# Performance work log

Hardware: AMD Instinct MI355X
Metric: run time of the kernel (lower is better)

The kernel has to match this reference:

```python
import jax, jax.numpy as jnp
import numpy as np

N_NODES = 100000


def _graph_conv(x, W, b, src, dst, n_nodes):
    # DGL GraphConv, norm='both', weight applied before aggregation (in>out).
    E = src.shape[0]
    ones = jnp.ones((E,), dtype=x.dtype)
    out_deg = jax.ops.segment_sum(ones, src, num_segments=n_nodes)
    in_deg = jax.ops.segment_sum(ones, dst, num_segments=n_nodes)
    out_norm = jnp.clip(out_deg, 1.0, None) ** -0.5  # [N]
    in_norm = jnp.clip(in_deg, 1.0, None) ** -0.5    # [N]
    h = (x * out_norm[:, None]) @ W                  # [N, out] dense GEMM first
    msg = h[src]                                     # gather  [E, out]
    agg = jax.ops.segment_sum(msg, dst, num_segments=n_nodes)  # scatter-add
    return agg * in_norm[:, None] + b


def setup_inputs() -> dict:
    key = jax.random.key(0)
    k1, k2, k3, k4, k5 = jax.random.split(key, 5)
    E = 1600000
    features = jax.random.normal(k1, (N_NODES, 128), dtype=jnp.float32)
    src = jax.random.randint(k2, (E,), 0, N_NODES, dtype=jnp.int64)
    dst = jax.random.randint(k3, (E,), 0, N_NODES, dtype=jnp.int64)
    W1 = jax.random.normal(k4, (128, 64), dtype=jnp.float32) * (1.0 / np.sqrt(128))
    b1 = jnp.zeros((64,), dtype=jnp.float32)
    W2 = jax.random.normal(k5, (64, 32), dtype=jnp.float32) * (1.0 / np.sqrt(64))
    b2 = jnp.zeros((32,), dtype=jnp.float32)
    return {"features": features, "src": src, "dst": dst,
            "W1": W1, "b1": b1, "W2": W2, "b2": b2}


def reference(features, src, dst, W1, b1, W2, b2):
    x = jax.nn.relu(_graph_conv(features, W1, b1, src, dst, N_NODES))
    x = _graph_conv(x, W2, b2, src, dst, N_NODES)
    return x
```

## Files before the change

kernel.cpp:

```cpp
#include <hip/hip_runtime.h>
#include <hip/hip_bf16.h>


#define BSH 7
#define BNODES 128
#define SRCMASK 0x1FFFF
#define CAP 2560
#define CHUNK 4096

__device__ __forceinline__ unsigned short f2bf(float f) {
    unsigned int u = __float_as_uint(f);
    return (unsigned short)((u + 0x7FFFu + ((u >> 16) & 1u)) >> 16);
}

__global__ __launch_bounds__(1024) void k_place(const int* __restrict__ src,
        const int* __restrict__ dst, int* __restrict__ ebuf,
        unsigned char* __restrict__ sbuf, int* __restrict__ offs,
        int* __restrict__ soffs, int E) {
    __shared__ int lh[800], s[800];
    int t = threadIdx.x;
    int e0 = blockIdx.x * CHUNK;
    int e1 = min(e0 + CHUNK, E);
    if (t < 800) lh[t] = 0;
    __syncthreads();
    for (int i = e0 + t; i < e1; i += 1024) {
        atomicAdd(&lh[dst[i] >> BSH], 0x10000);
        atomicAdd(&lh[src[i] >> BSH], 1);
    }
    __syncthreads();
    if (t < 800) s[t] = lh[t];
    __syncthreads();
    for (int o = 1; o < 800; o <<= 1) {
        int u = (t < 800 && t >= o) ? s[t - o] : 0;
        __syncthreads();
        if (t < 800) s[t] += u;
        __syncthreads();
    }
    int obase = blockIdx.x * 801;
    if (t < 800) {
        int incl = s[t], c = lh[t];
        int bd = (incl >> 16) - (c >> 16);
        int bs = (incl & 0xFFFF) - (c & 0xFFFF);
        offs[obase + t] = bd;
        soffs[obase + t] = bs;
        s[t] = (bd << 16) | bs;
    }
    if (t == 0) { offs[obase + 800] = e1 - e0; soffs[obase + 800] = e1 - e0; }
    __syncthreads();
    for (int i = e0 + t; i < e1; i += 1024) {
        int sv = src[i], d = dst[i];
        int pd = atomicAdd(&s[d >> BSH], 0x10000) >> 16;
        ebuf[e0 + pd] = sv | ((d & (BNODES - 1)) << 17);
        int ps = atomicAdd(&s[sv >> BSH], 1) & 0xFFFF;
        sbuf[e0 + ps] = (unsigned char)(sv & (BNODES - 1));
    }
}

__global__ __launch_bounds__(1024) void k_sort2(const int* __restrict__ ebuf,
        const unsigned char* __restrict__ sbuf, const int* __restrict__ offs,
        const int* __restrict__ soffs, int* __restrict__ csrc,
        int* __restrict__ ostart, int* __restrict__ oend,
        float* __restrict__ nI, float* __restrict__ nO, int n, int NBLK) {
    __shared__ int cnt[BNODES], cur[BNODES], s[BNODES], scnt[BNODES];
    __shared__ int segst[400], segen[400], sst[400], sen[400];
    int t = threadIdx.x, b = blockIdx.x;
    if (t < NBLK) {
        segst[t] = t * CHUNK + offs[t * 801 + b];
        segen[t] = t * CHUNK + offs[t * 801 + b + 1];
        sst[t]   = t * CHUNK + soffs[t * 801 + b];
        sen[t]   = t * CHUNK + soffs[t * 801 + b + 1];
    }
    if (t < BNODES) { cnt[t] = 0; scnt[t] = 0; }
    __syncthreads();
    int grp = t >> 3, ln = t & 7;
    for (int sg = grp; sg < NBLK; sg += 128) {
        int en = segen[sg];
        for (int i = segst[sg] + ln; i < en; i += 8)
            atomicAdd(&cnt[ebuf[i] >> 17], 1);
        int en2 = sen[sg];
        for (int i = sst[sg] + ln; i < en2; i += 8)
            atomicAdd(&scnt[sbuf[i]], 1);
    }
    __syncthreads();
    if (t < BNODES) s[t] = cnt[t];
    __syncthreads();
    for (int o = 1; o < BNODES; o <<= 1) {
        int u = (t < BNODES && t >= o) ? s[t - o] : 0;
        __syncthreads();
        if (t < BNODES) s[t] += u;
        __syncthreads();
    }
    if (t < BNODES) {
        int e0 = b * CAP;
        int st = e0 + s[t] - cnt[t];
        cur[t] = st;
        int g = b * BNODES + t;
        if (g < n) {
            ostart[g] = st;
            oend[g] = e0 + s[t];
            nI[g] = rsqrtf(fmaxf((float)cnt[t], 1.0f));
            nO[g] = rsqrtf(fmaxf((float)scnt[t], 1.0f));
        }
    }
    __syncthreads();
    for (int sg = grp; sg < NBLK; sg += 128) {
        int en = segen[sg];
        for (int i = segst[sg] + ln; i < en; i += 8) {
            int p = ebuf[i];
            int pos = atomicAdd(&cur[p >> 17], 1);
            csrc[pos] = p & SRCMASK;
        }
    }
}

__global__ __launch_bounds__(256) void k_gemm1(const float* __restrict__ x,
                        const float* __restrict__ W1, const float* __restrict__ nO,
                        unsigned short* __restrict__ h1, int n) {
    __shared__ float sX[64 * 132];
    __shared__ float sW[128 * 64];
    const int t = threadIdx.x;
    {
        const float4* W4 = (const float4*)W1;
        float4* sW4 = (float4*)sW;
#pragma unroll
        for (int i = 0; i < 8; i++) sW4[t + 256 * i] = W4[t + 256 * i];
    }
    const int rowbase = blockIdx.x * 64;
    {
        const float4* x4 = (const float4*)x;
        float4* sX4 = (float4*)sX;
#pragma unroll
        for (int i = 0; i < 8; i++) {
            int f = t + 256 * i;
            int row = f >> 5, kc = f & 31;
            int grow = rowbase + row;
            float4 v = make_float4(0.f, 0.f, 0.f, 0.f);
            if (grow < n) v = x4[(size_t)grow * 32 + kc];
            sX4[row * 33 + kc] = v;
        }
    }
    __syncthreads();
    const int lane = t & 63, wv = t >> 6;
    const int rg = lane >> 2, cg = lane & 3;
    const int c0 = wv * 16 + cg * 4;
    float acc[4][4] = {};
    for (int kk = 0; kk < 128; kk += 4) {
        float xr[4][4], wr[4][4];
#pragma unroll
        for (int i = 0; i < 4; i++)
            *(float4*)xr[i] = *(const float4*)&sX[(rg + 16 * i) * 132 + kk];
#pragma unroll
        for (int j = 0; j < 4; j++)
            *(float4*)wr[j] = *(const float4*)&sW[(kk + j) * 64 + c0];
#pragma unroll
        for (int j = 0; j < 4; j++)
#pragma unroll
            for (int i = 0; i < 4; i++)
#pragma unroll
                for (int c = 0; c < 4; c++)
                    acc[i][c] = fmaf(xr[i][j], wr[j][c], acc[i][c]);
    }
#pragma unroll
    for (int i = 0; i < 4; i++) {
        int grow = rowbase + rg + 16 * i;
        if (grow < n) {
            float nf = nO[grow];
            ushort4 o;
            o.x = f2bf(acc[i][0] * nf); o.y = f2bf(acc[i][1] * nf);
            o.z = f2bf(acc[i][2] * nf); o.w = f2bf(acc[i][3] * nf);
            *(ushort4*)&h1[(size_t)grow * 64 + c0] = o;
        }
    }
}

__global__ void k_agg64(const unsigned short* __restrict__ h,
                        const int* __restrict__ csrc,
                        const int* __restrict__ ostart, const int* __restrict__ oend,
                        const float* __restrict__ nI, const float* __restrict__ b1,
                        float* __restrict__ x2, int n) {
    int node = blockIdx.x * 4 + (threadIdx.x >> 6);
    int lane = threadIdx.x & 63;
    if (node >= n) return;
    int s0 = ostart[node], s1 = oend[node];
    int sub = lane >> 4;
    int c4 = (lane & 15) * 4;
    float a0 = 0.f, a1 = 0.f, a2 = 0.f, a3 = 0.f;
    float d0 = 0.f, d1 = 0.f, d2 = 0.f, d3 = 0.f;
    int e = s0;
    for (; e + 7 < s1; e += 8) {
        int p0 = csrc[e + sub];
        int p1 = csrc[e + 4 + sub];
        uint2 u0 = *(const uint2*)&h[(size_t)p0 * 64 + c4];
        uint2 u1 = *(const uint2*)&h[(size_t)p1 * 64 + c4];
        a0 += __uint_as_float(u0.x << 16);
        a1 += __uint_as_float(u0.x & 0xFFFF0000u);
        a2 += __uint_as_float(u0.y << 16);
        a3 += __uint_as_float(u0.y & 0xFFFF0000u);
        d0 += __uint_as_float(u1.x << 16);
        d1 += __uint_as_float(u1.x & 0xFFFF0000u);
        d2 += __uint_as_float(u1.y << 16);
        d3 += __uint_as_float(u1.y & 0xFFFF0000u);
    }
    for (; e < s1; e += 4) {
        if (e + sub < s1) {
            int p = csrc[e + sub];
            uint2 u = *(const uint2*)&h[(size_t)p * 64 + c4];
            a0 += __uint_as_float(u.x << 16);
            a1 += __uint_as_float(u.x & 0xFFFF0000u);
            a2 += __uint_as_float(u.y << 16);
            a3 += __uint_as_float(u.y & 0xFFFF0000u);
        }
    }
    a0 += d0; a1 += d1; a2 += d2; a3 += d3;
    a0 += __shfl(a0, lane ^ 16, 64);
    a1 += __shfl(a1, lane ^ 16, 64);
    a2 += __shfl(a2, lane ^ 16, 64);
    a3 += __shfl(a3, lane ^ 16, 64);
    a0 += __shfl(a0, lane ^ 32, 64);
    a1 += __shfl(a1, lane ^ 32, 64);
    a2 += __shfl(a2, lane ^ 32, 64);
    a3 += __shfl(a3, lane ^ 32, 64);
    if (sub == 0) {
        float ni = nI[node];
        float4 o;
        o.x = fmaxf(fmaf(a0, ni, b1[c4 + 0]), 0.f);
        o.y = fmaxf(fmaf(a1, ni, b1[c4 + 1]), 0.f);
        o.z = fmaxf(fmaf(a2, ni, b1[c4 + 2]), 0.f);
        o.w = fmaxf(fmaf(a3, ni, b1[c4 + 3]), 0.f);
        *(float4*)&x2[(size_t)node * 64 + c4] = o;
    }
}

__global__ __launch_bounds__(256) void k_gemm2(const float* __restrict__ x2,
                        const float* __restrict__ W2, const float* __restrict__ nO,
                        unsigned short* __restrict__ h2, int n) {
    __shared__ float sX[128 * 68];
    __shared__ float sW[64 * 32];
    const int t = threadIdx.x;
    {
        const float4* W4 = (const float4*)W2;
        float4* sW4 = (float4*)sW;
#pragma unroll
        for (int i = 0; i < 2; i++) sW4[t + 256 * i] = W4[t + 256 * i];
    }
    const int rowbase = blockIdx.x * 128;
    {
        const float4* x4 = (const float4*)x2;
        float4* sX4 = (float4*)sX;
#pragma unroll
        for (int i = 0; i < 8; i++) {
            int f = t + 256 * i;
            int row = f >> 4, kc = f & 15;
            int grow = rowbase + row;
            float4 v = make_float4(0.f, 0.f, 0.f, 0.f);
            if (grow < n) v = x4[(size_t)grow * 16 + kc];
            sX4[row * 17 + kc] = v;
        }
    }
    __syncthreads();
    const int lane = t & 63, wv = t >> 6;
    const int whalf = wv >> 1, chalf = wv & 1;
    const int rg = lane >> 2, cg = lane & 3;
    const int c0 = chalf * 16 + cg * 4;
    const int rloc = whalf * 64 + rg;
    float acc[4][4] = {};
    for (int kk = 0; kk < 64; kk += 4) {
        float xr[4][4], wr[4][4];
#pragma unroll
        for (int i = 0; i < 4; i++)
            *(float4*)xr[i] = *(const float4*)&sX[(rloc + 16 * i) * 68 + kk];
#pragma unroll
        for (int j = 0; j < 4; j++)
            *(float4*)wr[j] = *(const float4*)&sW[(kk + j) * 32 + c0];
#pragma unroll
        for (int j = 0; j < 4; j++)
#pragma unroll
            for (int i = 0; i < 4; i++)
#pragma unroll
                for (int c = 0; c < 4; c++)
                    acc[i][c] = fmaf(xr[i][j], wr[j][c], acc[i][c]);
    }
#pragma unroll
    for (int i = 0; i < 4; i++) {
        int grow = rowbase + rloc + 16 * i;
        if (grow < n) {
            float nf = nO[grow];
            ushort4 o;
            o.x = f2bf(acc[i][0] * nf); o.y = f2bf(acc[i][1] * nf);
            o.z = f2bf(acc[i][2] * nf); o.w = f2bf(acc[i][3] * nf);
            *(ushort4*)&h2[(size_t)grow * 32 + c0] = o;
        }
    }
}

__global__ void k_agg32(const unsigned short* __restrict__ h,
                        const int* __restrict__ csrc,
                        const int* __restrict__ ostart, const int* __restrict__ oend,
                        const float* __restrict__ nI, const float* __restrict__ b2,
                        float* __restrict__ out, int n) {
    int node = blockIdx.x * 4 + (threadIdx.x >> 6);
    int lane = threadIdx.x & 63;
    if (node >= n) return;
    int s0 = ostart[node], s1 = oend[node];
    int sub = lane >> 3;
    int c4 = (lane & 7) * 4;
    float a0 = 0.f, a1 = 0.f, a2 = 0.f, a3 = 0.f;
    float d0 = 0.f, d1 = 0.f, d2 = 0.f, d3 = 0.f;
    int e = s0;
    for (; e + 15 < s1; e += 16) {
        int p0 = csrc[e + sub];
        int p1 = csrc[e + 8 + sub];
        uint2 u0 = *(const uint2*)&h[(size_t)p0 * 32 + c4];
        uint2 u1 = *(const uint2*)&h[(size_t)p1 * 32 + c4];
        a0 += __uint_as_float(u0.x << 16);
        a1 += __uint_as_float(u0.x & 0xFFFF0000u);
        a2 += __uint_as_float(u0.y << 16);
        a3 += __uint_as_float(u0.y & 0xFFFF0000u);
        d0 += __uint_as_float(u1.x << 16);
        d1 += __uint_as_float(u1.x & 0xFFFF0000u);
        d2 += __uint_as_float(u1.y << 16);
        d3 += __uint_as_float(u1.y & 0xFFFF0000u);
    }
    for (; e < s1; e += 8) {
        if (e + sub < s1) {
            int p = csrc[e + sub];
            uint2 u = *(const uint2*)&h[(size_t)p * 32 + c4];
            a0 += __uint_as_float(u.x << 16);
            a1 += __uint_as_float(u.x & 0xFFFF0000u);
            a2 += __uint_as_float(u.y << 16);
            a3 += __uint_as_float(u.y & 0xFFFF0000u);
        }
    }
    a0 += d0; a1 += d1; a2 += d2; a3 += d3;
    a0 += __shfl(a0, lane ^ 8, 64);
    a1 += __shfl(a1, lane ^ 8, 64);
    a2 += __shfl(a2, lane ^ 8, 64);
    a3 += __shfl(a3, lane ^ 8, 64);
    a0 += __shfl(a0, lane ^ 16, 64);
    a1 += __shfl(a1, lane ^ 16, 64);
    a2 += __shfl(a2, lane ^ 16, 64);
    a3 += __shfl(a3, lane ^ 16, 64);
    a0 += __shfl(a0, lane ^ 32, 64);
    a1 += __shfl(a1, lane ^ 32, 64);
    a2 += __shfl(a2, lane ^ 32, 64);
    a3 += __shfl(a3, lane ^ 32, 64);
    if (sub == 0) {
        float ni = nI[node];
        float4 o;
        o.x = fmaf(a0, ni, b2[c4 + 0]);
        o.y = fmaf(a1, ni, b2[c4 + 1]);
        o.z = fmaf(a2, ni, b2[c4 + 2]);
        o.w = fmaf(a3, ni, b2[c4 + 3]);
        *(float4*)&out[(size_t)node * 32 + c4] = o;
    }
}

extern "C" void kernel_launch(void* const* d_in, const int* in_sizes, int n_in,
                              void* d_out, int out_size, void* d_ws, size_t ws_size,
                              hipStream_t stream) {
    const float* x   = (const float*)d_in[0];
    const int*   src = (const int*)d_in[1];
    const int*   dst = (const int*)d_in[2];
    const float* W1  = (const float*)d_in[3];
    const float* b1  = (const float*)d_in[4];
    const float* W2  = (const float*)d_in[5];
    const float* b2  = (const float*)d_in[6];
    float* out = (float*)d_out;

    const int N = in_sizes[0] / 128;
    const int E = in_sizes[1];
    const int NB = (N + BNODES - 1) / BNODES;
    const int NBLK = (E + CHUNK - 1) / CHUNK;

    char* wsb = (char*)d_ws;
    float* nO     = (float*)wsb;  wsb += (size_t)N * 4;
    float* nI     = (float*)wsb;  wsb += (size_t)N * 4;
    int*   ostart = (int*)wsb;    wsb += (size_t)N * 4;
    int*   oend   = (int*)wsb;    wsb += (size_t)N * 4;
    int*   csrc   = (int*)wsb;    wsb += (size_t)NB * CAP * 4;
    int*   offs   = (int*)wsb;    wsb += (size_t)NBLK * 801 * 4;
    unsigned short* h1 = (unsigned short*)wsb;
                                  wsb += (size_t)N * 64 * 2;
    float* x2     = (float*)wsb;  wsb += (size_t)N * 64 * 4;
    unsigned short* h2 = h1;
    int*   ebuf   = (int*)x2;
    unsigned char* sbuf = (unsigned char*)(ebuf) + (size_t)E * 4;
    int*   soffs  = (int*)(sbuf + (size_t)E);

    k_place<<<NBLK, 1024, 0, stream>>>(src, dst, ebuf, sbuf, offs, soffs, E);
    k_sort2<<<NB, 1024, 0, stream>>>(ebuf, sbuf, offs, soffs, csrc,
                                     ostart, oend, nI, nO, N, NBLK);

    k_gemm1<<<(N + 63) / 64, 256, 0, stream>>>(x, W1, nO, h1, N);
    k_agg64<<<(N + 3) / 4, 256, 0, stream>>>(h1, csrc, ostart, oend, nI, b1, x2, N);

    k_gemm2<<<(N + 127) / 128, 256, 0, stream>>>(x2, W2, nO, h2, N);
    k_agg32<<<(N + 3) / 4, 256, 0, stream>>>(h2, csrc, ostart, oend, nI, b2, out, N);
}
```

Before: 297.0 us.

## Split layer-1 features into four column slices and aggregate each slice separately

```diff
diff --git a/kernel.cpp b/kernel.cpp
--- a/kernel.cpp
+++ b/kernel.cpp
@@ -7,6 +7,8 @@
 #define SRCMASK 0x1FFFF
 #define CAP 2560
 #define CHUNK 4096
+
+typedef float f4v __attribute__((ext_vector_type(4)));
 
 __device__ __forceinline__ unsigned short f2bf(float f) {
     unsigned int u = __float_as_uint(f);
@@ -160,6 +162,7 @@
                 for (int c = 0; c < 4; c++)
                     acc[i][c] = fmaf(xr[i][j], wr[j][c], acc[i][c]);
     }
+    const size_t pl = (size_t)n * 16;
 #pragma unroll
     for (int i = 0; i < 4; i++) {
         int grow = rowbase + rg + 16 * i;
@@ -168,30 +171,32 @@
             ushort4 o;
             o.x = f2bf(acc[i][0] * nf); o.y = f2bf(acc[i][1] * nf);
             o.z = f2bf(acc[i][2] * nf); o.w = f2bf(acc[i][3] * nf);
-            *(ushort4*)&h1[(size_t)grow * 64 + c0] = o;
-        }
-    }
-}
-
-__global__ void k_agg64(const unsigned short* __restrict__ h,
-                        const int* __restrict__ csrc,
-                        const int* __restrict__ ostart, const int* __restrict__ oend,
-                        const float* __restrict__ nI, const float* __restrict__ b1,
-                        float* __restrict__ x2, int n) {
-    int node = blockIdx.x * 4 + (threadIdx.x >> 6);
-    int lane = threadIdx.x & 63;
+            *(ushort4*)&h1[(size_t)wv * pl + (size_t)grow * 16 + cg * 4] = o;
+        }
+    }
+}
+
+__global__ void k_agg64s(const unsigned short* __restrict__ h,
+                         const int* __restrict__ csrc,
+                         const int* __restrict__ ostart, const int* __restrict__ oend,
+                         const float* __restrict__ nI, const float* __restrict__ b1,
+                         float* __restrict__ x2, int n) {
+    const int s = blockIdx.x & 3;
+    const int node = (blockIdx.x >> 2) * 4 + (threadIdx.x >> 6);
+    const int lane = threadIdx.x & 63;
     if (node >= n) return;
     int s0 = ostart[node], s1 = oend[node];
-    int sub = lane >> 4;
-    int c4 = (lane & 15) * 4;
+    const int sub = lane >> 2;
+    const int cl = lane & 3;
+    const uint2* hs = (const uint2*)h + (size_t)s * n * 4;
     float a0 = 0.f, a1 = 0.f, a2 = 0.f, a3 = 0.f;
     float d0 = 0.f, d1 = 0.f, d2 = 0.f, d3 = 0.f;
     int e = s0;
-    for (; e + 7 < s1; e += 8) {
-        int p0 = csrc[e + sub];
-        int p1 = csrc[e + 4 + sub];
-        uint2 u0 = *(const uint2*)&h[(size_t)p0 * 64 + c4];
-        uint2 u1 = *(const uint2*)&h[(size_t)p1 * 64 + c4];
+    for (; e + 31 < s1; e += 32) {
+        int p0 = __builtin_nontemporal_load(csrc + e + sub);
+        int p1 = __builtin_nontemporal_load(csrc + e + 16 + sub);
+        uint2 u0 = hs[(size_t)p0 * 4 + cl];
+        uint2 u1 = hs[(size_t)p1 * 4 + cl];
         a0 += __uint_as_float(u0.x << 16);
         a1 += __uint_as_float(u0.x & 0xFFFF0000u);
         a2 += __uint_as_float(u0.y << 16);
@@ -201,10 +206,10 @@
         d2 += __uint_as_float(u1.y << 16);
         d3 += __uint_as_float(u1.y & 0xFFFF0000u);
     }
-    for (; e < s1; e += 4) {
+    for (; e < s1; e += 16) {
         if (e + sub < s1) {
-            int p = csrc[e + sub];
-            uint2 u = *(const uint2*)&h[(size_t)p * 64 + c4];
+            int p = __builtin_nontemporal_load(csrc + e + sub);
+            uint2 u = hs[(size_t)p * 4 + cl];
             a0 += __uint_as_float(u.x << 16);
             a1 += __uint_as_float(u.x & 0xFFFF0000u);
             a2 += __uint_as_float(u.y << 16);
@@ -212,6 +217,14 @@
         }
     }
     a0 += d0; a1 += d1; a2 += d2; a3 += d3;
+    a0 += __shfl(a0, lane ^ 4, 64);
+    a1 += __shfl(a1, lane ^ 4, 64);
+    a2 += __shfl(a2, lane ^ 4, 64);
+    a3 += __shfl(a3, lane ^ 4, 64);
+    a0 += __shfl(a0, lane ^ 8, 64);
+    a1 += __shfl(a1, lane ^ 8, 64);
+    a2 += __shfl(a2, lane ^ 8, 64);
+    a3 += __shfl(a3, lane ^ 8, 64);
     a0 += __shfl(a0, lane ^ 16, 64);
     a1 += __shfl(a1, lane ^ 16, 64);
     a2 += __shfl(a2, lane ^ 16, 64);
@@ -222,12 +235,14 @@
     a3 += __shfl(a3, lane ^ 32, 64);
     if (sub == 0) {
         float ni = nI[node];
-        float4 o;
-        o.x = fmaxf(fmaf(a0, ni, b1[c4 + 0]), 0.f);
-        o.y = fmaxf(fmaf(a1, ni, b1[c4 + 1]), 0.f);
-        o.z = fmaxf(fmaf(a2, ni, b1[c4 + 2]), 0.f);
-        o.w = fmaxf(fmaf(a3, ni, b1[c4 + 3]), 0.f);
-        *(float4*)&x2[(size_t)node * 64 + c4] = o;
+        const float* bb = b1 + s * 16 + cl * 4;
+        f4v o;
+        o[0] = fmaxf(fmaf(a0, ni, bb[0]), 0.f);
+        o[1] = fmaxf(fmaf(a1, ni, bb[1]), 0.f);
+        o[2] = fmaxf(fmaf(a2, ni, bb[2]), 0.f);
+        o[3] = fmaxf(fmaf(a3, ni, bb[3]), 0.f);
+        __builtin_nontemporal_store(o,
+            (f4v*)(x2 + (size_t)s * n * 16 + (size_t)node * 16 + cl * 4));
     }
 }
 
@@ -244,6 +259,7 @@
         for (int i = 0; i < 2; i++) sW4[t + 256 * i] = W4[t + 256 * i];
     }
     const int rowbase = blockIdx.x * 128;
+    const size_t n4 = (size_t)n * 4;
     {
         const float4* x4 = (const float4*)x2;
         float4* sX4 = (float4*)sX;
@@ -253,7 +269,8 @@
             int row = f >> 4, kc = f & 15;
             int grow = rowbase + row;
             float4 v = make_float4(0.f, 0.f, 0.f, 0.f);
-            if (grow < n) v = x4[(size_t)grow * 16 + kc];
+            if (grow < n)
+                v = x4[(size_t)(kc >> 2) * n4 + (size_t)grow * 4 + (kc & 3)];
             sX4[row * 17 + kc] = v;
         }
     }
@@ -392,7 +409,8 @@
                                      ostart, oend, nI, nO, N, NBLK);
 
     k_gemm1<<<(N + 63) / 64, 256, 0, stream>>>(x, W1, nO, h1, N);
-    k_agg64<<<(N + 3) / 4, 256, 0, stream>>>(h1, csrc, ostart, oend, nI, b1, x2, N);
+    k_agg64s<<<((N + 3) / 4) * 4, 256, 0, stream>>>(h1, csrc, ostart, oend,
+                                                    nI, b1, x2, N);
 
     k_gemm2<<<(N + 127) / 128, 256, 0, stream>>>(x2, W2, nO, h2, N);
     k_agg32<<<(N + 3) / 4, 256, 0, stream>>>(h2, csrc, ostart, oend, nI, b2, out, N);
```

After: 387.6 us. +30.5%, slower.
